# Optimization experiments

Measured on AMD Instinct MI355X. Metric: run time of the kernel, lower is better.

The kernel has to match this reference:

```python
import jax, jax.numpy as jnp
import numpy as np

NUM_HEADS = 12
DIM_HEAD = 64
EPS = 1e-5


def _layer_norm(x, g, b):
    m = jnp.mean(x, axis=-1, keepdims=True)
    v = jnp.mean(jnp.square(x - m), axis=-1, keepdims=True)
    return (x - m) * jax.lax.rsqrt(v + EPS) * g + b


def setup_inputs() -> dict:
    key = jax.random.key(0)
    ks = jax.random.split(key, 3)
    B, S, L, D = 1, 128, 256, NUM_HEADS * DIM_HEAD
    x = jax.random.normal(ks[0], (B, S, L, D), dtype=jnp.float32)
    w_row = jax.random.normal(ks[1], (3 * D, D), dtype=jnp.float32) * 0.02
    b_row = jnp.zeros((3 * D,), dtype=jnp.float32)
    w_col = jax.random.normal(ks[2], (3 * D, D), dtype=jnp.float32) * 0.02
    b_col = jnp.zeros((3 * D,), dtype=jnp.float32)
    g1 = jnp.ones((D,), dtype=jnp.float32)
    beta1 = jnp.zeros((D,), dtype=jnp.float32)
    g2 = jnp.ones((D,), dtype=jnp.float32)
    beta2 = jnp.zeros((D,), dtype=jnp.float32)
    return {"x": x, "w_row": w_row, "b_row": b_row, "w_col": w_col,
            "b_col": b_col, "g1": g1, "beta1": beta1, "g2": g2, "beta2": beta2}


def reference(x, w_row, b_row, w_col, b_col, g1, beta1, g2, beta2):
    B, S, L, D = x.shape
    H, dh = NUM_HEADS, DIM_HEAD

    def qkv(inp, w, b):
        p = inp @ w.T + b                      # [B,S,L,3D]
        q, k, v = jnp.split(p, 3, axis=-1)
        rs = lambda t: t.reshape(B, S, L, H, dh)
        return rs(q), rs(k), rs(v)

    # --- tied row attention: logits summed over S (no 1/sqrt(dh) scaling, as in source) ---
    q, k, v = qkv(x, w_row, b_row)
    row_attn = jnp.einsum('bsihc,bsjhc->bhij', q, k)      # [B,H,L,L]
    row_attn = jax.nn.softmax(row_attn, axis=-1)
    row_out = jnp.einsum('bhij,bsjhd->bsihd', row_attn, v).reshape(B, S, L, D)
    out = _layer_norm(x + row_out, g1, beta1)

    # --- column attention: softmax over the j (sequence) axis ---
    q, k, v = qkv(out, w_col, b_col)
    col_attn = jnp.einsum('bilhc,bjlhc->bhijl', q, k)     # [B,H,S,S,L]
    col_attn = jax.nn.softmax(col_attn, axis=-2)
    col_out = jnp.einsum('bhijl,bjlhd->bilhd', col_attn, v).reshape(B, S, L, D)
    out = _layer_norm(out + col_out, g2, beta2)
    return out
```

## Files before the change

### kernel.cpp

```cpp
#include <hip/hip_runtime.h>

#define S_DIM 128
#define L_DIM 256
#define D_DIM 768
#define H_DIM 12
#define TD    2304
#define NROW  32768
#define KDIM  768
#define LN_EPS 1e-5f

typedef unsigned short u16;
typedef unsigned int   u32;
typedef _Float16 f16;
typedef _Float16 f16x8 __attribute__((ext_vector_type(8)));
typedef _Float16 f16x4 __attribute__((ext_vector_type(4)));
typedef float    f32x4 __attribute__((ext_vector_type(4)));

#define WS_QT_OFF     0
#define WS_KT_OFF     50331648
#define WS_VT_OFF     100663296
#define WS_P_OFF      0
#define WS_LPART_OFF  150994944
#define WS_PT_OFF     176160768
#define WS_XH_OFF     177733632
#define WS_WRH_OFF    228065280
#define WS_WCH_OFF    231604224

__device__ __forceinline__ void gload_lds16(const void* g, void* l) {
    __builtin_amdgcn_global_load_lds((const __attribute__((address_space(1))) void*)g,
                                     (__attribute__((address_space(3))) void*)l, 16, 0, 0);
}

__global__ __launch_bounds__(256)
void cvt_f32_f16(const float* __restrict__ in, f16* __restrict__ out)
{
    int i = blockIdx.x * 256 + threadIdx.x;
    float4 v = ((const float4*)in)[i];
    f16x4 o; o.x = (f16)v.x; o.y = (f16)v.y; o.z = (f16)v.z; o.w = (f16)v.w;
    ((f16x4*)out)[i] = o;
}

#define MFMA_PROLOG(KROW)                                                     \
    __shared__ f16 As[128 * 32];                                              \
    __shared__ f16 Bs[128 * 32];                                              \
    const int tid  = threadIdx.x;                                             \
    const int lane = tid & 63;                                                \
    const int w    = tid >> 6;                                                \
    const int wr   = (w >> 1) * 64;                                           \
    const int wc   = (w & 1) * 64;                                            \
    const int lm   = lane & 15;                                               \
    const int q    = lane >> 4;                                               \
    size_t soff[2];                                                           \
    int    ldsc[2];                                                           \
    _Pragma("unroll")                                                         \
    for (int t = 0; t < 2; ++t) {                                             \
        int c  = w * 128 + t * 64 + lane;                                     \
        int m  = c >> 2;                                                      \
        int gj = (c & 3) ^ ((m >> 1) & 3);                                    \
        soff[t] = (size_t)m * (KROW) + gj * 8;                                \
        ldsc[t] = (w * 128 + t * 64) * 8;                                     \
    }                                                                         \
    int chA[4], chB[4];                                                       \
    _Pragma("unroll")                                                         \
    for (int t = 0; t < 4; ++t) {                                             \
        int ma = wr + t * 16 + lm;                                            \
        chA[t] = ma * 4 + (q ^ ((ma >> 1) & 3));                              \
        int mb = wc + t * 16 + lm;                                            \
        chB[t] = mb * 4 + (q ^ ((mb >> 1) & 3));                              \
    }                                                                         \
    f32x4 acc[4][4];                                                          \
    _Pragma("unroll")                                                         \
    for (int i = 0; i < 4; ++i)                                               \
        _Pragma("unroll")                                                     \
        for (int j = 0; j < 4; ++j) acc[i][j] = (f32x4)0.f;

#define MFMA_KLOOP(baseA, baseB, KLEN)                                        \
    for (int k0 = 0; k0 < (KLEN); k0 += 32) {                                 \
        _Pragma("unroll")                                                     \
        for (int t = 0; t < 2; ++t) {                                         \
            gload_lds16((baseA) + soff[t] + k0, &As[ldsc[t]]);                \
            gload_lds16((baseB) + soff[t] + k0, &Bs[ldsc[t]]);                \
        }                                                                     \
        __syncthreads();                                                      \
        f16x8 af[4], bf[4];                                                   \
        _Pragma("unroll")                                                     \
        for (int t = 0; t < 4; ++t) af[t] = *(const f16x8*)&As[chA[t] * 8];   \
        _Pragma("unroll")                                                     \
        for (int t = 0; t < 4; ++t) bf[t] = *(const f16x8*)&Bs[chB[t] * 8];   \
        _Pragma("unroll")                                                     \
        for (int mt = 0; mt < 4; ++mt)                                        \
            _Pragma("unroll")                                                 \
            for (int nt = 0; nt < 4; ++nt)                                    \
                acc[mt][nt] = __builtin_amdgcn_mfma_f32_16x16x32_f16(         \
                    af[mt], bf[nt], acc[mt][nt], 0, 0, 0);                    \
        __syncthreads();                                                      \
    }

#define R3_WAIT_(N) asm volatile("s_waitcnt vmcnt(" #N ")" ::: "memory")
#define R3_WAIT(N)  R3_WAIT_(N)

#define R3_PROLOG()                                                           \
    __shared__ f16 As0[256 * 64];                                             \
    __shared__ f16 As1[256 * 64];                                             \
    __shared__ f16 As2[256 * 64];                                             \
    __shared__ f16 Bs0[192 * 64];                                             \
    __shared__ f16 Bs1[192 * 64];                                             \
    const int tid  = threadIdx.x;                                             \
    const int lane = tid & 63;                                                \
    const int w    = tid >> 6;                                                \
    const int wr   = (w >> 1) * 64;                                           \
    const int wc   = (w & 1) * 96;                                            \
    const int lm   = lane & 15;                                               \
    const int q    = lane >> 4;                                               \
    size_t soffA[4];                                                          \
    _Pragma("unroll")                                                         \
    for (int i = 0; i < 4; ++i) {                                             \
        int c = i * 512 + tid;                                                \
        int r = c >> 3;                                                       \
        int j = (c & 7) ^ (r & 7);                                            \
        soffA[i] = (size_t)r * KDIM + j * 8;                                  \
    }                                                                         \
    size_t soffB[3];                                                          \
    _Pragma("unroll")                                                         \
    for (int i = 0; i < 3; ++i) {                                             \
        int c = i * 512 + tid;                                                \
        int r = c >> 3;                                                       \
        int j = (c & 7) ^ (r & 7);                                            \
        soffB[i] = (size_t)r * KDIM + j * 8;                                  \
    }                                                                         \
    f32x4 acc[4][6];                                                          \
    _Pragma("unroll")                                                         \
    for (int i = 0; i < 4; ++i)                                               \
        _Pragma("unroll")                                                     \
        for (int j = 0; j < 6; ++j) acc[i][j] = (f32x4)0.f;

#define R3_STAGE_A(Ad, kk)                                                    \
    _Pragma("unroll")                                                         \
    for (int i = 0; i < 4; ++i)                                               \
        gload_lds16(baseA + soffA[i] + (size_t)(kk) * 64,                     \
                    &Ad[(i * 512 + w * 64) * 8]);

#define R3_STAGE_B(Bd, kk)                                                    \
    _Pragma("unroll")                                                         \
    for (int i = 0; i < 3; ++i)                                               \
        gload_lds16(baseB + soffB[i] + (size_t)(kk) * 64,                     \
                    &Bd[(i * 512 + w * 64) * 8]);

#define R3_FRAG(buf, row, ks)                                                 \
    (*(const f16x8*)&buf[(size_t)(row) * 64 +                                 \
                         ((((ks) * 4 + q) ^ ((row) & 7)) * 8)])

#define R3_COMPUTE(Ab, Bb)                                                    \
    _Pragma("unroll")                                                         \
    for (int ks = 0; ks < 2; ++ks) {                                          \
        f16x8 af[4], bf[6];                                                   \
        _Pragma("unroll")                                                     \
        for (int mt = 0; mt < 4; ++mt)                                        \
            af[mt] = R3_FRAG(Ab, wr + mt * 16 + lm, ks);                      \
        _Pragma("unroll")                                                     \
        for (int nt = 0; nt < 6; ++nt)                                        \
            bf[nt] = R3_FRAG(Bb, wc + nt * 16 + lm, ks);                      \
        __builtin_amdgcn_s_setprio(1);                                        \
        _Pragma("unroll")                                                     \
        for (int mt = 0; mt < 4; ++mt)                                        \
            _Pragma("unroll")                                                 \
            for (int nt = 0; nt < 6; ++nt)                                    \
                acc[mt][nt] = __builtin_amdgcn_mfma_f32_16x16x32_f16(         \
                    af[mt], bf[nt], acc[mt][nt], 0, 0, 0);                    \
        __builtin_amdgcn_s_setprio(0);                                        \
    }

#define R3_TILE(Ab, Bb, SB, Bn, kb, SA, An, ka, WN)                           \
    R3_WAIT(WN);                                                              \
    __builtin_amdgcn_s_barrier();                                             \
    __builtin_amdgcn_sched_barrier(0);                                        \
    if (SB) { R3_STAGE_B(Bn, kb) }                                            \
    if (SA) { R3_STAGE_A(An, ka) }                                            \
    R3_COMPUTE(Ab, Bb)

#define R3_KLOOP768()                                                         \
    R3_STAGE_A(As0, 0)                                                        \
    R3_STAGE_B(Bs0, 0)                                                        \
    R3_STAGE_A(As1, 1)                                                        \
    R3_TILE(As0, Bs0, 1, Bs1, 1,  1, As2, 2,  4)                              \
    R3_TILE(As1, Bs1, 1, Bs0, 2,  1, As0, 3,  4)                              \
    R3_TILE(As2, Bs0, 1, Bs1, 3,  1, As1, 4,  4)                              \
    R3_TILE(As0, Bs1, 1, Bs0, 4,  1, As2, 5,  4)                              \
    R3_TILE(As1, Bs0, 1, Bs1, 5,  1, As0, 6,  4)                              \
    R3_TILE(As2, Bs1, 1, Bs0, 6,  1, As1, 7,  4)                              \
    R3_TILE(As0, Bs0, 1, Bs1, 7,  1, As2, 8,  4)                              \
    R3_TILE(As1, Bs1, 1, Bs0, 8,  1, As0, 9,  4)                              \
    R3_TILE(As2, Bs0, 1, Bs1, 9,  1, As1, 10, 4)                              \
    R3_TILE(As0, Bs1, 1, Bs0, 10, 1, As2, 11, 4)                              \
    R3_TILE(As1, Bs0, 1, Bs1, 11, 0, As0, 0,  4)                              \
    R3_TILE(As2, Bs1, 0, Bs0, 0,  0, As0, 0,  0)

#define R3_SWIZZLE()                                                          \
    const int wg   = blockIdx.y * 12 + blockIdx.x;                            \
    const int swz  = (wg & 7) * 192 + (wg >> 3);                              \
    const int row0 = (swz / 12) * 256;                                        \
    const int col0 = (swz % 12) * 192;

__global__ __launch_bounds__(512, 2)
void mfma_gemm_qkv(const f16* __restrict__ A, const f16* __restrict__ W,
                   const float* __restrict__ bias, f16* __restrict__ C)
{
    R3_SWIZZLE()
    R3_PROLOG()
    const f16* baseA = A + (size_t)row0 * KDIM;
    const f16* baseB = W + (size_t)col0 * KDIM;
    R3_KLOOP768()

    float bv[6];
#pragma unroll
    for (int nt = 0; nt < 6; ++nt) bv[nt] = bias[col0 + wc + nt * 16 + lm];
#pragma unroll
    for (int mt = 0; mt < 4; ++mt) {
        int grow = row0 + wr + mt * 16 + q * 4;
#pragma unroll
        for (int nt = 0; nt < 6; ++nt) {
            int gcol = col0 + wc + nt * 16 + lm;
#pragma unroll
            for (int r = 0; r < 4; ++r)
                C[(size_t)(grow + r) * TD + gcol] = (f16)(acc[mt][nt][r] + bv[nt]);
        }
    }
}

__global__ __launch_bounds__(512, 2)
void mfma_gemm_row(const f16* __restrict__ A, const f16* __restrict__ W,
                   const float* __restrict__ bias,
                   f16* __restrict__ qt, f16* __restrict__ kt,
                   f16* __restrict__ vt)
{
    R3_SWIZZLE()
    R3_PROLOG()
    const f16* baseA = A + (size_t)row0 * KDIM;
    const f16* baseB = W + (size_t)col0 * KDIM;
    R3_KLOOP768()

    if (col0 < 1536) {
        f16* dst = (col0 < 768) ? qt : kt;
        const int cbase = (col0 < 768) ? col0 : col0 - 768;
#pragma unroll
        for (int nt = 0; nt < 6; ++nt) {
            int gcol = cbase + wc + nt * 16 + lm;
            int h = gcol >> 6, c = gcol & 63;
            float b = bias[col0 + wc + nt * 16 + lm];
#pragma unroll
            for (int mt = 0; mt < 4; ++mt) {
                int n0 = row0 + wr + mt * 16 + q * 4;
#pragma unroll
                for (int r = 0; r < 4; ++r) {
                    int n = n0 + r;
                    int s = n >> 8, ii = n & 255;
                    dst[(((size_t)h * 256 + ii) * 128 + s) * 64 + c] =
                        (f16)(acc[mt][nt][r] + b);
                }
            }
        }
    } else {
#pragma unroll
        for (int nt = 0; nt < 6; ++nt) {
            int gcol = col0 + wc + nt * 16 + lm;
            int vcol = gcol - 1536;
            int h = vcol >> 6, d = vcol & 63;
            float b = bias[gcol];
#pragma unroll
            for (int mt = 0; mt < 4; ++mt) {
                int n0 = row0 + wr + mt * 16 + q * 4;
                int s = n0 >> 8, j0 = n0 & 255;
                f16x4 pack;
#pragma unroll
                for (int r = 0; r < 4; ++r) pack[r] = (f16)(acc[mt][nt][r] + b);
                *(f16x4*)&vt[((((size_t)h * 128 + s) * 64 + d) << 8) + j0] = pack;
            }
        }
    }
}

__global__ __launch_bounds__(256)
void row_logits_mfma(const f16* __restrict__ qt, const f16* __restrict__ kt,
                     float* __restrict__ lpart)
{
    const int i0 = blockIdx.y * 128;
    const int j0 = blockIdx.x * 128;
    const int h  = blockIdx.z >> 3;
    const int sp = blockIdx.z & 7;
    MFMA_PROLOG(8192)
    const f16* baseA = qt + ((size_t)h * 256 + i0) * 8192 + sp * 1024;
    const f16* baseB = kt + ((size_t)h * 256 + j0) * 8192 + sp * 1024;
    MFMA_KLOOP(baseA, baseB, 1024)

    float* outp = lpart + (size_t)(sp * 12 + h) * 65536;
#pragma unroll
    for (int mt = 0; mt < 4; ++mt) {
        int grow = i0 + wr + mt * 16 + q * 4;
#pragma unroll
        for (int nt = 0; nt < 4; ++nt) {
            int gcol = j0 + wc + nt * 16 + lm;
#pragma unroll
            for (int r = 0; r < 4; ++r)
                outp[(size_t)(grow + r) * 256 + gcol] = acc[mt][nt][r];
        }
    }
}

__global__ __launch_bounds__(256)
void softmax256_8(const float* __restrict__ lpart, f16* __restrict__ pt)
{
    __shared__ float red[256];
    const int t = threadIdx.x;
    const size_t idx = (size_t)blockIdx.x * 256 + t;
    const size_t P = (size_t)12 * 65536;
    float v = 0.f;
#pragma unroll
    for (int p8 = 0; p8 < 8; ++p8) v += lpart[idx + p8 * P];
    red[t] = v; __syncthreads();
    for (int w = 128; w > 0; w >>= 1) { if (t < w) red[t] = fmaxf(red[t], red[t+w]); __syncthreads(); }
    float m = red[0];
    __syncthreads();
    float e = __expf(v - m);
    red[t] = e; __syncthreads();
    for (int w = 128; w > 0; w >>= 1) { if (t < w) red[t] += red[t+w]; __syncthreads(); }
    pt[idx] = (f16)(e / red[0]);
}

__global__ __launch_bounds__(256)
void row_pv_mfma(const f16* __restrict__ pt, const f16* __restrict__ vt,
                 f16* __restrict__ rout)
{
    const int n0t = blockIdx.x * 128;
    const int i0  = blockIdx.y * 128;
    const int h   = blockIdx.z;
    MFMA_PROLOG(256)
    const f16* baseA = pt + (size_t)h * 65536 + (size_t)i0 * 256;
    const f16* baseB = vt + ((size_t)h * 8192 + n0t) * 256;
    MFMA_KLOOP(baseA, baseB, 256)

#pragma unroll
    for (int mt = 0; mt < 4; ++mt) {
        int irow = i0 + wr + mt * 16 + q * 4;
#pragma unroll
        for (int nt = 0; nt < 4; ++nt) {
            int n = n0t + wc + nt * 16 + lm;
            int s = n >> 6, d = n & 63;
#pragma unroll
            for (int r = 0; r < 4; ++r)
                rout[(size_t)(s * 256 + irow + r) * D_DIM + h * 64 + d] =
                    (f16)acc[mt][nt][r];
        }
    }
}

__global__ __launch_bounds__(256)
void add_ln_out16(const f16* __restrict__ x16, const f16* __restrict__ r,
                  const float* __restrict__ g, const float* __restrict__ beta,
                  f16* __restrict__ out16)
{
    __shared__ float red[256];
    const int n = blockIdx.x, t = threadIdx.x;
    const f16* xp = x16 + (size_t)n * D_DIM;
    const f16* rp = r   + (size_t)n * D_DIM;
    float v[3]; float s = 0.f;
#pragma unroll
    for (int e = 0; e < 3; ++e) { v[e] = (float)xp[t + e*256] + (float)rp[t + e*256]; s += v[e]; }
    red[t] = s; __syncthreads();
    for (int w = 128; w > 0; w >>= 1) { if (t < w) red[t] += red[t+w]; __syncthreads(); }
    float mean = red[0] * (1.f/768.f);
    __syncthreads();
    float sq = 0.f;
#pragma unroll
    for (int e = 0; e < 3; ++e) { float d = v[e] - mean; sq += d*d; }
    red[t] = sq; __syncthreads();
    for (int w = 128; w > 0; w >>= 1) { if (t < w) red[t] += red[t+w]; __syncthreads(); }
    float rstd = rsqrtf(red[0] * (1.f/768.f) + LN_EPS);
#pragma unroll
    for (int e = 0; e < 3; ++e) {
        int idx = t + e*256;
        out16[(size_t)n * D_DIM + idx] = (f16)((v[e] - mean) * rstd * g[idx] + beta[idx]);
    }
}

__global__ __launch_bounds__(256)
void add_ln_in16(const f16* __restrict__ x16, float* __restrict__ r,
                 const float* __restrict__ g, const float* __restrict__ beta)
{
    __shared__ float red[256];
    const int n = blockIdx.x, t = threadIdx.x;
    const f16*   xp = x16 + (size_t)n * D_DIM;
    float*       rp = r   + (size_t)n * D_DIM;
    float v[3]; float s = 0.f;
#pragma unroll
    for (int e = 0; e < 3; ++e) { v[e] = (float)xp[t + e*256] + rp[t + e*256]; s += v[e]; }
    red[t] = s; __syncthreads();
    for (int w = 128; w > 0; w >>= 1) { if (t < w) red[t] += red[t+w]; __syncthreads(); }
    float mean = red[0] * (1.f/768.f);
    __syncthreads();
    float sq = 0.f;
#pragma unroll
    for (int e = 0; e < 3; ++e) { float d = v[e] - mean; sq += d*d; }
    red[t] = sq; __syncthreads();
    for (int w = 128; w > 0; w >>= 1) { if (t < w) red[t] += red[t+w]; __syncthreads(); }
    float rstd = rsqrtf(red[0] * (1.f/768.f) + LN_EPS);
#pragma unroll
    for (int e = 0; e < 3; ++e) {
        int idx = t + e*256;
        rp[idx] = (v[e] - mean) * rstd * g[idx] + beta[idx];
    }
}

__global__ __launch_bounds__(256, 3)
void col_attn_mfma(const f16* __restrict__ p, float* __restrict__ cout)
{
    __shared__ char smem[54272];
    f16* Qs = (f16*)smem;
    f16* Ks = (f16*)(smem + 18432);
    f16* Ps = (f16*)smem;
    f16* Vt = (f16*)(smem + 36864);

    const int tid  = threadIdx.x;
    const int lane = tid & 63;
    const int w    = tid >> 6;
    const int lm   = lane & 15;
    const int q    = lane >> 4;
    const int l = blockIdx.x, h = blockIdx.y;
    const int ib = w * 32;

    {
        const int r  = tid >> 1;
        const int hc = (tid & 1) * 32;
        const f16* rowp = p + (size_t)(r * 256 + l) * TD + h * 64 + hc;
#pragma unroll
        for (int cc = 0; cc < 4; ++cc)
            *(float4*)&Qs[r * 72 + hc + cc * 8] = *(const float4*)(rowp + cc * 8);
#pragma unroll
        for (int cc = 0; cc < 4; ++cc)
            *(float4*)&Ks[r * 72 + hc + cc * 8] = *(const float4*)(rowp + 768 + cc * 8);
#pragma unroll
        for (int cc = 0; cc < 4; ++cc) {
            union { float4 f; u16 u[8]; } vb;
            vb.f = *(const float4*)(rowp + 1536 + cc * 8);
#pragma unroll
            for (int e = 0; e < 8; ++e) {
                int d = hc + cc * 8 + e;
                ((u16*)Vt)[d * 136 + r] = vb.u[e];
            }
        }
    }
    __syncthreads();

    f32x4 acc[2][8];
#pragma unroll
    for (int mt = 0; mt < 2; ++mt)
#pragma unroll
        for (int nt = 0; nt < 8; ++nt) acc[mt][nt] = (f32x4)0.f;
#pragma unroll
    for (int ks = 0; ks < 2; ++ks) {
        f16x8 af[2];
#pragma unroll
        for (int mt = 0; mt < 2; ++mt)
            af[mt] = *(const f16x8*)&Qs[(ib + mt * 16 + lm) * 72 + ks * 32 + q * 8];
#pragma unroll
        for (int nt = 0; nt < 8; ++nt) {
            f16x8 bf = *(const f16x8*)&Ks[(nt * 16 + lm) * 72 + ks * 32 + q * 8];
#pragma unroll
            for (int mt = 0; mt < 2; ++mt)
                acc[mt][nt] = __builtin_amdgcn_mfma_f32_16x16x32_f16(
                    af[mt], bf, acc[mt][nt], 0, 0, 0);
        }
    }
    __syncthreads();

    float inv_sum[2][4];
#pragma unroll
    for (int mt = 0; mt < 2; ++mt) {
#pragma unroll
        for (int r = 0; r < 4; ++r) {
            float m = acc[mt][0][r];
#pragma unroll
            for (int nt = 1; nt < 8; ++nt) m = fmaxf(m, acc[mt][nt][r]);
#pragma unroll
            for (int d = 1; d < 16; d <<= 1) m = fmaxf(m, __shfl_xor(m, d));
            float s = 0.f;
#pragma unroll
            for (int nt = 0; nt < 8; ++nt) {
                float e = __expf(acc[mt][nt][r] - m);
                acc[mt][nt][r] = e; s += e;
            }
#pragma unroll
            for (int d = 1; d < 16; d <<= 1) s += __shfl_xor(s, d);
            inv_sum[mt][r] = 1.f / s;
        }
        const int irow = ib + mt * 16 + q * 4;
#pragma unroll
        for (int nt = 0; nt < 8; ++nt) {
            const int jj = nt * 16 + lm;
#pragma unroll
            for (int r = 0; r < 4; ++r)
                Ps[(irow + r) * 136 + jj] = (f16)acc[mt][nt][r];
        }
    }
    __syncthreads();

    f32x4 acc2[2][4];
#pragma unroll
    for (int mt = 0; mt < 2; ++mt)
#pragma unroll
        for (int nt = 0; nt < 4; ++nt) acc2[mt][nt] = (f32x4)0.f;
#pragma unroll
    for (int ks = 0; ks < 4; ++ks) {
        f16x8 pf[2];
#pragma unroll
        for (int mt = 0; mt < 2; ++mt)
            pf[mt] = *(const f16x8*)&Ps[(ib + mt * 16 + lm) * 136 + ks * 32 + q * 8];
#pragma unroll
        for (int nt = 0; nt < 4; ++nt) {
            f16x8 vf = *(const f16x8*)&Vt[(nt * 16 + lm) * 136 + ks * 32 + q * 8];
#pragma unroll
            for (int mt = 0; mt < 2; ++mt)
                acc2[mt][nt] = __builtin_amdgcn_mfma_f32_16x16x32_f16(
                    pf[mt], vf, acc2[mt][nt], 0, 0, 0);
        }
    }

#pragma unroll
    for (int mt = 0; mt < 2; ++mt) {
        const int irow = ib + mt * 16 + q * 4;
#pragma unroll
        for (int nt = 0; nt < 4; ++nt) {
            const int d = nt * 16 + lm;
#pragma unroll
            for (int r = 0; r < 4; ++r)
                cout[(size_t)((irow + r) * 256 + l) * D_DIM + h * 64 + d] =
                    acc2[mt][nt][r] * inv_sum[mt][r];
        }
    }
}

extern "C" void kernel_launch(void* const* d_in, const int* in_sizes, int n_in,
                              void* d_out, int out_size, void* d_ws, size_t ws_size,
                              hipStream_t stream)
{
    const float* x     = (const float*)d_in[0];
    const float* w_row = (const float*)d_in[1];
    const float* b_row = (const float*)d_in[2];
    const float* w_col = (const float*)d_in[3];
    const float* b_col = (const float*)d_in[4];
    const float* g1    = (const float*)d_in[5];
    const float* be1   = (const float*)d_in[6];
    const float* g2    = (const float*)d_in[7];
    const float* be2   = (const float*)d_in[8];
    float* out = (float*)d_out;

    char* ws = (char*)d_ws;
    f16*   qt     = (f16*)(ws + WS_QT_OFF);
    f16*   kt     = (f16*)(ws + WS_KT_OFF);
    f16*   vt     = (f16*)(ws + WS_VT_OFF);
    f16*   p      = (f16*)(ws + WS_P_OFF);
    float* lpart  = (float*)(ws + WS_LPART_OFF);
    f16*   pt     = (f16*)(ws + WS_PT_OFF);
    f16*   xh     = (f16*)(ws + WS_XH_OFF);
    f16*   wrh    = (f16*)(ws + WS_WRH_OFF);
    f16*   wch    = (f16*)(ws + WS_WCH_OFF);
    f16*   rout_h = qt;

    cvt_f32_f16<<<NROW * D_DIM / 1024, 256, 0, stream>>>(x, xh);
    cvt_f32_f16<<<TD * D_DIM / 1024, 256, 0, stream>>>(w_row, wrh);
    cvt_f32_f16<<<TD * D_DIM / 1024, 256, 0, stream>>>(w_col, wch);
    mfma_gemm_row<<<dim3(12, 128), 512, 0, stream>>>(xh, wrh, b_row, qt, kt, vt);
    row_logits_mfma<<<dim3(2, 2, 96), 256, 0, stream>>>(qt, kt, lpart);
    softmax256_8<<<H_DIM * L_DIM, 256, 0, stream>>>(lpart, pt);
    row_pv_mfma<<<dim3(64, 2, H_DIM), 256, 0, stream>>>(pt, vt, rout_h);
    add_ln_out16<<<NROW, 256, 0, stream>>>(xh, rout_h, g1, be1, xh);
    mfma_gemm_qkv<<<dim3(12, 128), 512, 0, stream>>>(xh, wch, b_col, p);
    col_attn_mfma<<<dim3(L_DIM, H_DIM), 256, 0, stream>>>(p, out);
    add_ln_in16<<<NROW, 256, 0, stream>>>(xh, out, g2, be2);
}
```

Before: 688.9 us.

## Use wave-per-row reductions for softmax and layernorm; transpose col QKV output layout

Rewrites softmax and both add+layernorm kernels so that one 64-lane wave handles a whole row. Each uses vectorized loads and stores and reduces with xor shuffles, removing the shared-memory tree reductions and their many barriers. The column QKV GEMM now writes its output in an l-major, s-minor row order, so the column-attention kernel reads 128 consecutive rows for a fixed l instead of rows strided by 256. This makes the column-attention loads contiguous, but the GEMM epilogue stores are now scattered across rows.

Measured after the change: 645.0 us. -6.4%, faster.

```diff
diff --git a/kernel.cpp b/kernel.cpp
--- a/kernel.cpp
+++ b/kernel.cpp
@@ -211,18 +211,20 @@
     const f16* baseB = W + (size_t)col0 * KDIM;
     R3_KLOOP768()
 
+    const int srow = row0 >> 8;
     float bv[6];
 #pragma unroll
     for (int nt = 0; nt < 6; ++nt) bv[nt] = bias[col0 + wc + nt * 16 + lm];
 #pragma unroll
     for (int mt = 0; mt < 4; ++mt) {
-        int grow = row0 + wr + mt * 16 + q * 4;
+        int lrow = wr + mt * 16 + q * 4;
 #pragma unroll
         for (int nt = 0; nt < 6; ++nt) {
             int gcol = col0 + wc + nt * 16 + lm;
 #pragma unroll
             for (int r = 0; r < 4; ++r)
-                C[(size_t)(grow + r) * TD + gcol] = (f16)(acc[mt][nt][r] + bv[nt]);
+                C[(size_t)((lrow + r) * 128 + srow) * TD + gcol] =
+                    (f16)(acc[mt][nt][r] + bv[nt]);
         }
     }
 }
@@ -309,21 +311,29 @@
 __global__ __launch_bounds__(256)
 void softmax256_8(const float* __restrict__ lpart, f16* __restrict__ pt)
 {
-    __shared__ float red[256];
-    const int t = threadIdx.x;
-    const size_t idx = (size_t)blockIdx.x * 256 + t;
+    const int row  = blockIdx.x * 4 + (threadIdx.x >> 6);
+    const int lane = threadIdx.x & 63;
+    const size_t idx = (size_t)row * 256 + lane * 4;
     const size_t P = (size_t)12 * 65536;
-    float v = 0.f;
-#pragma unroll
-    for (int p8 = 0; p8 < 8; ++p8) v += lpart[idx + p8 * P];
-    red[t] = v; __syncthreads();
-    for (int w = 128; w > 0; w >>= 1) { if (t < w) red[t] = fmaxf(red[t], red[t+w]); __syncthreads(); }
-    float m = red[0];
-    __syncthreads();
-    float e = __expf(v - m);
-    red[t] = e; __syncthreads();
-    for (int w = 128; w > 0; w >>= 1) { if (t < w) red[t] += red[t+w]; __syncthreads(); }
-    pt[idx] = (f16)(e / red[0]);
+    float4 v = *(const float4*)&lpart[idx];
+#pragma unroll
+    for (int p8 = 1; p8 < 8; ++p8) {
+        float4 u = *(const float4*)&lpart[idx + p8 * P];
+        v.x += u.x; v.y += u.y; v.z += u.z; v.w += u.w;
+    }
+    float m = fmaxf(fmaxf(v.x, v.y), fmaxf(v.z, v.w));
+#pragma unroll
+    for (int d = 1; d < 64; d <<= 1) m = fmaxf(m, __shfl_xor(m, d));
+    float e0 = __expf(v.x - m), e1 = __expf(v.y - m);
+    float e2 = __expf(v.z - m), e3 = __expf(v.w - m);
+    float s = e0 + e1 + e2 + e3;
+#pragma unroll
+    for (int d = 1; d < 64; d <<= 1) s += __shfl_xor(s, d);
+    float inv = 1.f / s;
+    f16x4 o;
+    o[0] = (f16)(e0 * inv); o[1] = (f16)(e1 * inv);
+    o[2] = (f16)(e2 * inv); o[3] = (f16)(e3 * inv);
+    *(f16x4*)&pt[idx] = o;
 }
 
 __global__ __launch_bounds__(256)
@@ -358,56 +368,104 @@
                   const float* __restrict__ g, const float* __restrict__ beta,
                   f16* __restrict__ out16)
 {
-    __shared__ float red[256];
-    const int n = blockIdx.x, t = threadIdx.x;
-    const f16* xp = x16 + (size_t)n * D_DIM;
-    const f16* rp = r   + (size_t)n * D_DIM;
-    float v[3]; float s = 0.f;
-#pragma unroll
-    for (int e = 0; e < 3; ++e) { v[e] = (float)xp[t + e*256] + (float)rp[t + e*256]; s += v[e]; }
-    red[t] = s; __syncthreads();
-    for (int w = 128; w > 0; w >>= 1) { if (t < w) red[t] += red[t+w]; __syncthreads(); }
-    float mean = red[0] * (1.f/768.f);
-    __syncthreads();
+    const int n    = blockIdx.x * 4 + (threadIdx.x >> 6);
+    const int lane = threadIdx.x & 63;
+    const size_t base = (size_t)n * D_DIM;
+    const int oa = lane * 8, ob = 512 + lane * 4;
+
+    f16x8 xa = *(const f16x8*)&x16[base + oa];
+    f16x8 ra = *(const f16x8*)&r[base + oa];
+    f16x4 xb = *(const f16x4*)&x16[base + ob];
+    f16x4 rb = *(const f16x4*)&r[base + ob];
+
+    float va[8], vb[4]; float s = 0.f;
+#pragma unroll
+    for (int e = 0; e < 8; ++e) { va[e] = (float)xa[e] + (float)ra[e]; s += va[e]; }
+#pragma unroll
+    for (int e = 0; e < 4; ++e) { vb[e] = (float)xb[e] + (float)rb[e]; s += vb[e]; }
+#pragma unroll
+    for (int d = 1; d < 64; d <<= 1) s += __shfl_xor(s, d);
+    float mean = s * (1.f / 768.f);
     float sq = 0.f;
 #pragma unroll
-    for (int e = 0; e < 3; ++e) { float d = v[e] - mean; sq += d*d; }
-    red[t] = sq; __syncthreads();
-    for (int w = 128; w > 0; w >>= 1) { if (t < w) red[t] += red[t+w]; __syncthreads(); }
-    float rstd = rsqrtf(red[0] * (1.f/768.f) + LN_EPS);
-#pragma unroll
-    for (int e = 0; e < 3; ++e) {
-        int idx = t + e*256;
-        out16[(size_t)n * D_DIM + idx] = (f16)((v[e] - mean) * rstd * g[idx] + beta[idx]);
-    }
+    for (int e = 0; e < 8; ++e) { float dd = va[e] - mean; sq += dd * dd; }
+#pragma unroll
+    for (int e = 0; e < 4; ++e) { float dd = vb[e] - mean; sq += dd * dd; }
+#pragma unroll
+    for (int d = 1; d < 64; d <<= 1) sq += __shfl_xor(sq, d);
+    float rstd = rsqrtf(sq * (1.f / 768.f) + LN_EPS);
+
+    float4 g0 = *(const float4*)&g[oa], g1 = *(const float4*)&g[oa + 4];
+    float4 b0 = *(const float4*)&beta[oa], b1 = *(const float4*)&beta[oa + 4];
+    float4 g2 = *(const float4*)&g[ob], b2 = *(const float4*)&beta[ob];
+    float ga[8] = {g0.x,g0.y,g0.z,g0.w,g1.x,g1.y,g1.z,g1.w};
+    float ba[8] = {b0.x,b0.y,b0.z,b0.w,b1.x,b1.y,b1.z,b1.w};
+    float gb[4] = {g2.x,g2.y,g2.z,g2.w};
+    float bb[4] = {b2.x,b2.y,b2.z,b2.w};
+
+    f16x8 outa; f16x4 outb;
+#pragma unroll
+    for (int e = 0; e < 8; ++e)
+        outa[e] = (f16)((va[e] - mean) * rstd * ga[e] + ba[e]);
+#pragma unroll
+    for (int e = 0; e < 4; ++e)
+        outb[e] = (f16)((vb[e] - mean) * rstd * gb[e] + bb[e]);
+    *(f16x8*)&out16[base + oa] = outa;
+    *(f16x4*)&out16[base + ob] = outb;
 }
 
 __global__ __launch_bounds__(256)
 void add_ln_in16(const f16* __restrict__ x16, float* __restrict__ r,
                  const float* __restrict__ g, const float* __restrict__ beta)
 {
-    __shared__ float red[256];
-    const int n = blockIdx.x, t = threadIdx.x;
-    const f16*   xp = x16 + (size_t)n * D_DIM;
-    float*       rp = r   + (size_t)n * D_DIM;
-    float v[3]; float s = 0.f;
-#pragma unroll
-    for (int e = 0; e < 3; ++e) { v[e] = (float)xp[t + e*256] + rp[t + e*256]; s += v[e]; }
-    red[t] = s; __syncthreads();
-    for (int w = 128; w > 0; w >>= 1) { if (t < w) red[t] += red[t+w]; __syncthreads(); }
-    float mean = red[0] * (1.f/768.f);
-    __syncthreads();
+    const int n    = blockIdx.x * 4 + (threadIdx.x >> 6);
+    const int lane = threadIdx.x & 63;
+    const size_t base = (size_t)n * D_DIM;
+    const int oa = lane * 8, ob = 512 + lane * 4;
+
+    f16x8 xa = *(const f16x8*)&x16[base + oa];
+    float4 r0 = *(const float4*)&r[base + oa];
+    float4 r1 = *(const float4*)&r[base + oa + 4];
+    f16x4 xb = *(const f16x4*)&x16[base + ob];
+    float4 r2 = *(const float4*)&r[base + ob];
+    float rav[8] = {r0.x,r0.y,r0.z,r0.w,r1.x,r1.y,r1.z,r1.w};
+    float rbv[4] = {r2.x,r2.y,r2.z,r2.w};
+
+    float va[8], vb[4]; float s = 0.f;
+#pragma unroll
+    for (int e = 0; e < 8; ++e) { va[e] = (float)xa[e] + rav[e]; s += va[e]; }
+#pragma unroll
+    for (int e = 0; e < 4; ++e) { vb[e] = (float)xb[e] + rbv[e]; s += vb[e]; }
+#pragma unroll
+    for (int d = 1; d < 64; d <<= 1) s += __shfl_xor(s, d);
+    float mean = s * (1.f / 768.f);
     float sq = 0.f;
 #pragma unroll
-    for (int e = 0; e < 3; ++e) { float d = v[e] - mean; sq += d*d; }
-    red[t] = sq; __syncthreads();
-    for (int w = 128; w > 0; w >>= 1) { if (t < w) red[t] += red[t+w]; __syncthreads(); }
-    float rstd = rsqrtf(red[0] * (1.f/768.f) + LN_EPS);
-#pragma unroll
-    for (int e = 0; e < 3; ++e) {
-        int idx = t + e*256;
-        rp[idx] = (v[e] - mean) * rstd * g[idx] + beta[idx];
-    }
+    for (int e = 0; e < 8; ++e) { float dd = va[e] - mean; sq += dd * dd; }
+#pragma unroll
+    for (int e = 0; e < 4; ++e) { float dd = vb[e] - mean; sq += dd * dd; }
+#pragma unroll
+    for (int d = 1; d < 64; d <<= 1) sq += __shfl_xor(sq, d);
+    float rstd = rsqrtf(sq * (1.f / 768.f) + LN_EPS);
+
+    float4 g0 = *(const float4*)&g[oa], g1 = *(const float4*)&g[oa + 4];
+    float4 b0 = *(const float4*)&beta[oa], b1 = *(const float4*)&beta[oa + 4];
+    float4 g2 = *(const float4*)&g[ob], b2 = *(const float4*)&beta[ob];
+    float ga[8] = {g0.x,g0.y,g0.z,g0.w,g1.x,g1.y,g1.z,g1.w};
+    float ba[8] = {b0.x,b0.y,b0.z,b0.w,b1.x,b1.y,b1.z,b1.w};
+    float gb[4] = {g2.x,g2.y,g2.z,g2.w};
+    float bb[4] = {b2.x,b2.y,b2.z,b2.w};
+
+    float4 o0, o1, o2;
+    o0.x = (va[0]-mean)*rstd*ga[0]+ba[0]; o0.y = (va[1]-mean)*rstd*ga[1]+ba[1];
+    o0.z = (va[2]-mean)*rstd*ga[2]+ba[2]; o0.w = (va[3]-mean)*rstd*ga[3]+ba[3];
+    o1.x = (va[4]-mean)*rstd*ga[4]+ba[4]; o1.y = (va[5]-mean)*rstd*ga[5]+ba[5];
+    o1.z = (va[6]-mean)*rstd*ga[6]+ba[6]; o1.w = (va[7]-mean)*rstd*ga[7]+ba[7];
+    o2.x = (vb[0]-mean)*rstd*gb[0]+bb[0]; o2.y = (vb[1]-mean)*rstd*gb[1]+bb[1];
+    o2.z = (vb[2]-mean)*rstd*gb[2]+bb[2]; o2.w = (vb[3]-mean)*rstd*gb[3]+bb[3];
+    *(float4*)&r[base + oa] = o0;
+    *(float4*)&r[base + oa + 4] = o1;
+    *(float4*)&r[base + ob] = o2;
 }
 
 __global__ __launch_bounds__(256, 3)
@@ -430,7 +488,7 @@
     {
         const int r  = tid >> 1;
         const int hc = (tid & 1) * 32;
-        const f16* rowp = p + (size_t)(r * 256 + l) * TD + h * 64 + hc;
+        const f16* rowp = p + (size_t)(l * 128 + r) * TD + h * 64 + hc;
 #pragma unroll
         for (int cc = 0; cc < 4; ++cc)
             *(float4*)&Qs[r * 72 + hc + cc * 8] = *(const float4*)(rowp + cc * 8);
@@ -570,10 +628,10 @@
     cvt_f32_f16<<<TD * D_DIM / 1024, 256, 0, stream>>>(w_col, wch);
     mfma_gemm_row<<<dim3(12, 128), 512, 0, stream>>>(xh, wrh, b_row, qt, kt, vt);
     row_logits_mfma<<<dim3(2, 2, 96), 256, 0, stream>>>(qt, kt, lpart);
-    softmax256_8<<<H_DIM * L_DIM, 256, 0, stream>>>(lpart, pt);
+    softmax256_8<<<H_DIM * L_DIM / 4, 256, 0, stream>>>(lpart, pt);
     row_pv_mfma<<<dim3(64, 2, H_DIM), 256, 0, stream>>>(pt, vt, rout_h);
-    add_ln_out16<<<NROW, 256, 0, stream>>>(xh, rout_h, g1, be1, xh);
+    add_ln_out16<<<NROW / 4, 256, 0, stream>>>(xh, rout_h, g1, be1, xh);
     mfma_gemm_qkv<<<dim3(12, 128), 512, 0, stream>>>(xh, wch, b_col, p);
     col_attn_mfma<<<dim3(L_DIM, H_DIM), 256, 0, stream>>>(p, out);
-    add_ln_in16<<<NROW, 256, 0, stream>>>(xh, out, g2, be2);
-}
+    add_ln_in16<<<NROW / 4, 256, 0, stream>>>(xh, out, g2, be2);
+}
```
